# Performance work log

Measured on AMD Instinct MI355X. Metric: run time of the kernel, lower is better.

The kernel has to match this reference:

```python
import jax, jax.numpy as jnp
import numpy as np

B, H, S, DK, DV = 2, 16, 2048, 64, 64

def setup_inputs() -> dict:
    key = jax.random.key(0)
    kq, kk, kv, km = jax.random.split(key, 4)
    q = jax.random.normal(kq, (B, H, S, DK), dtype=jnp.float32)
    k = jax.random.normal(kk, (B, H, S, DK), dtype=jnp.float32)
    v = jax.random.normal(kv, (B, H, S, DV), dtype=jnp.float32)
    mask = jax.random.randint(km, (B, H, S, S), 0, 2).astype(jnp.bool_)
    return {"q": q, "k": k, "v": v, "mask": mask}

def reference(q, k, v, mask):
    d_k = q.shape[-1]
    # scores: [B, H, Sq, Sk]
    scores = jnp.einsum('bhqd,bhkd->bhqk', q, k) / np.sqrt(d_k).astype(jnp.float32)
    scores = jnp.where(mask, jnp.float32(-1e9), scores)
    attn = jax.nn.softmax(scores, axis=-1)
    return jnp.einsum('bhqk,bhkd->bhqd', attn, v)
```

## Files before the change

kernel.cpp:

```cpp
#include <hip/hip_runtime.h>


#define LOG2E 1.4426950408889634f
#define QSCALE (0.125f * LOG2E)

typedef __attribute__((ext_vector_type(8))) short short8;
typedef __attribute__((ext_vector_type(4))) short short4v;
typedef __attribute__((ext_vector_type(4))) float f32x4;
typedef unsigned __attribute__((ext_vector_type(4))) uintv4;

constexpr int S = 2048, D = 64;

__device__ __forceinline__ short bf16rne(float x) {
  union { float f; unsigned u; } cv; cv.f = x;
  unsigned u = cv.u;
  u += 0x7fffu + ((u >> 16) & 1u);
  return (short)(u >> 16);
}

__device__ __forceinline__ void glds16(const void* g, void* l) {
  __builtin_amdgcn_global_load_lds(
      (const __attribute__((address_space(1))) void*)g,
      (__attribute__((address_space(3))) void*)l, 16, 0, 0);
}

__global__ void prep(const float* __restrict__ kp, const float* __restrict__ vp,
                     short* __restrict__ kb, short* __restrict__ vt,
                     const unsigned* __restrict__ m, int* __restrict__ flag) {
  const int b = blockIdx.x;
  const int tid = threadIdx.x;
  if (b == 0 && tid < 64) {
    unsigned v = m[tid];
    unsigned long long big = __ballot(v > 1u && v != 0x3F800000u);
    unsigned long long isf = __ballot(v == 0x3F800000u);
    if (tid == 0) *flag = (big != 0ull && isf == 0ull) ? 1 : 0;
  }
  if (b < 2048) {
    size_t i = ((size_t)b * 256 + tid) * 8;
    float4 a = *(const float4*)(kp + i);
    float4 c = *(const float4*)(kp + i + 4);
    short8 s;
    s[0] = bf16rne(a.x); s[1] = bf16rne(a.y); s[2] = bf16rne(a.z); s[3] = bf16rne(a.w);
    s[4] = bf16rne(c.x); s[5] = bf16rne(c.y); s[6] = bf16rne(c.z); s[7] = bf16rne(c.w);
    *(short8*)&kb[i] = s;
  } else {
    __shared__ float tile[64][65];
    const int bb = b - 2048;
    const int bh = bb >> 5, k0 = (bb & 31) * 64;
    const float* src = vp + ((size_t)(bh * S + k0)) * D;
#pragma unroll
    for (int i = 0; i < 4; ++i) {
      int row = i * 16 + (tid >> 4);
      int col = (tid & 15) * 4;
      float4 x = *(const float4*)(src + row * D + col);
      tile[row][col] = x.x; tile[row][col + 1] = x.y;
      tile[row][col + 2] = x.z; tile[row][col + 3] = x.w;
    }
    __syncthreads();
#pragma unroll
    for (int i = 0; i < 4; ++i) {
      int dim = i * 16 + (tid >> 4);
      int kb4 = (tid & 15) * 4;
      short4v s;
#pragma unroll
      for (int j = 0; j < 4; ++j) s[j] = bf16rne(tile[kb4 + j][dim]);
      *(short4v*)&vt[((size_t)(bh * D + dim)) * S + k0 + kb4] = s;
    }
  }
}

__launch_bounds__(256, 4)
__global__ void attn_fwd(const float* __restrict__ qp, const short* __restrict__ kb,
                         const short* __restrict__ vt, const void* __restrict__ mp,
                         float* __restrict__ op, const int* __restrict__ fmtp) {
  const int fmt  = *fmtp;
  const int tid  = threadIdx.x;
  const int lane = tid & 63;
  const int w    = tid >> 6;
  const int c    = lane & 15;
  const int quad = lane >> 4;
  const int cx   = c & 7;

  const int bh = blockIdx.x >> 5;
  const int q0 = (blockIdx.x & 31) * 64;

  __shared__ short ks[2][64 * 64];
  __shared__ short vs[2][64 * 64];
  __shared__ short pst[4][16 * 64];

  const float* qg = qp + ((size_t)(bh * S + q0 + w * 16 + c)) * D;
  short8 qB[2];
#pragma unroll
  for (int kk = 0; kk < 2; ++kk) {
    const float* p = qg + kk * 32 + quad * 8;
    float4 x = *(const float4*)(p);
    float4 y = *(const float4*)(p + 4);
    short8 f;
    f[0] = bf16rne(x.x * QSCALE); f[1] = bf16rne(x.y * QSCALE);
    f[2] = bf16rne(x.z * QSCALE); f[3] = bf16rne(x.w * QSCALE);
    f[4] = bf16rne(y.x * QSCALE); f[5] = bf16rne(y.y * QSCALE);
    f[6] = bf16rne(y.z * QSCALE); f[7] = bf16rne(y.w * QSCALE);
    qB[kk] = f;
  }

  f32x4 O[4];
#pragma unroll
  for (int t = 0; t < 4; ++t) O[t] = (f32x4){0.f, 0.f, 0.f, 0.f};
  float L = 0.f;

  const int rsub = lane >> 3;
  const int csw  = (lane & 7) ^ rsub;
  const short* kbase = kb + ((size_t)(bh * S)) * D;
  const short* vbase = vt + ((size_t)(bh * D)) * S;

  const int sw0 = ((quad    ) ^ cx) * 8;
  const int sw1 = ((quad | 4) ^ cx) * 8;

  const size_t mrow = ((size_t)(bh * S + q0 + w * 16 + c)) * S;

  uintv4  mr4[4];
  unsigned mr1[4];

  auto stage = [&](int it, int buf) {
    const int k0 = it * 64;
#pragma unroll
    for (int h2 = 0; h2 < 2; ++h2) {
      const int row = (h2 * 4 + w) * 8 + rsub;
      glds16(kbase + (size_t)(k0 + row) * 64 + csw * 8,
             (char*)&ks[buf][0] + (h2 * 4 + w) * 1024);
      glds16(vbase + (size_t)row * S + k0 + csw * 8,
             (char*)&vs[buf][0] + (h2 * 4 + w) * 1024);
    }
  };

  stage(0, 0);
  if (fmt == 1) {
    const unsigned char* mq = (const unsigned char*)mp + mrow + 4 * quad;
#pragma unroll
    for (int t = 0; t < 4; ++t)
      mr1[t] = __builtin_nontemporal_load((const unsigned*)(mq + 16 * t));
  } else {
    const unsigned* mq = (const unsigned*)mp + mrow + 4 * quad;
#pragma unroll
    for (int t = 0; t < 4; ++t)
      mr4[t] = __builtin_nontemporal_load((const uintv4*)(mq + 16 * t));
  }

  for (int it = 0; it < 32; ++it) {
    const int buf = it & 1;
    __syncthreads();

    if (it + 1 < 32) stage(it + 1, buf ^ 1);

    unsigned mb[4];
    if (fmt == 1) {
#pragma unroll
      for (int t = 0; t < 4; ++t) mb[t] = mr1[t];
    } else {
#pragma unroll
      for (int t = 0; t < 4; ++t) {
        uintv4 v = mr4[t];
        mb[t] = (v[0] ? 1u : 0u) | (v[1] ? 0x100u : 0u) |
                (v[2] ? 0x10000u : 0u) | (v[3] ? 0x1000000u : 0u);
      }
    }

    if (it + 1 < 32) {
      const int k1 = (it + 1) * 64;
      if (fmt == 1) {
        const unsigned char* mq = (const unsigned char*)mp + mrow + k1 + 4 * quad;
#pragma unroll
        for (int t = 0; t < 4; ++t)
          mr1[t] = __builtin_nontemporal_load((const unsigned*)(mq + 16 * t));
      } else {
        const unsigned* mq = (const unsigned*)mp + mrow + k1 + 4 * quad;
#pragma unroll
        for (int t = 0; t < 4; ++t)
          mr4[t] = __builtin_nontemporal_load((const uintv4*)(mq + 16 * t));
      }
    }

    float part = 0.f;
#pragma unroll
    for (int t = 0; t < 4; ++t) {
      short8 ka0 = *(const short8*)&ks[buf][(16 * t + c) * 64 + sw0];
      short8 ka1 = *(const short8*)&ks[buf][(16 * t + c) * 64 + sw1];
      f32x4 z = (f32x4){0.f, 0.f, 0.f, 0.f};
      z = __builtin_amdgcn_mfma_f32_16x16x32_bf16(ka0, qB[0], z, 0, 0, 0);
      z = __builtin_amdgcn_mfma_f32_16x16x32_bf16(ka1, qB[1], z, 0, 0, 0);
      short4v s4;
#pragma unroll
      for (int r = 0; r < 4; ++r) {
        float e = ((mb[t] >> (8 * r)) & 0xffu) ? 0.f : exp2f(z[r]);
        part += e;
        s4[r] = bf16rne(e);
      }
      *(short4v*)&pst[w][c * 64 + (((2 * t + (quad >> 1)) ^ cx) << 3) +
                         ((quad & 1) << 2)] = s4;
    }

    part += __shfl_xor(part, 16);
    part += __shfl_xor(part, 32);
    L += part;

    short8 pa0 = *(const short8*)&pst[w][c * 64 + ((quad ^ cx) << 3)];
    short8 pa1 = *(const short8*)&pst[w][c * 64 + (((quad | 4) ^ cx) << 3)];
#pragma unroll
    for (int t = 0; t < 4; ++t) {
      short8 vb0 = *(const short8*)&vs[buf][(16 * t + c) * 64 + sw0];
      short8 vb1 = *(const short8*)&vs[buf][(16 * t + c) * 64 + sw1];
      O[t] = __builtin_amdgcn_mfma_f32_16x16x32_bf16(pa0, vb0, O[t], 0, 0, 0);
      O[t] = __builtin_amdgcn_mfma_f32_16x16x32_bf16(pa1, vb1, O[t], 0, 0, 0);
    }
  }

#pragma unroll
  for (int r = 0; r < 4; ++r) {
    float Lr = __shfl(L, (lane & 48) | (quad * 4 + r));
    float inv = 1.f / Lr;
    const size_t ob = ((size_t)(bh * S + q0 + w * 16 + quad * 4 + r)) * D;
#pragma unroll
    for (int t = 0; t < 4; ++t) op[ob + 16 * t + c] = O[t][r] * inv;
  }
}

extern "C" void kernel_launch(void* const* d_in, const int* in_sizes, int n_in,
                              void* d_out, int out_size, void* d_ws, size_t ws_size,
                              hipStream_t stream) {
  const float* q = (const float*)d_in[0];
  const float* k = (const float*)d_in[1];
  const float* v = (const float*)d_in[2];
  const void*  m = d_in[3];

  short* kbuf = (short*)d_ws;
  short* vtb  = (short*)((char*)d_ws + (8u << 20));
  int* flag   = (int*)((char*)d_ws + (16u << 20));

  prep<<<3072, 256, 0, stream>>>(k, v, kbuf, vtb, (const unsigned*)m, flag);
  attn_fwd<<<1024, 256, 0, stream>>>(q, kbuf, vtb, m, (float*)d_out, flag);
}
```

Measured before the change: 757.8 us.

## Split key range across waves, load K/V fragments directly, merge partials via LDS

Each block's four waves now split into two query halves and two key halves. Each wave loads K and V^T fragments straight from global memory into registers instead of staging them in shared memory with async copies and a barrier every iteration. The P fragment is built in registers by permuting K rows so that no shared-memory round trip is needed. The two key-half partial outputs and row sums are combined through LDS at the end, and block IDs are swizzled for locality. This removes per-iteration barriers and LDS traffic but drops mask prefetching and double buffering, so it relies on caches and enough occupancy to hide global latency.

Measured after the change: 781.3 us. 3.1% more time.

```diff
diff --git a/kernel.cpp b/kernel.cpp
--- a/kernel.cpp
+++ b/kernel.cpp
@@ -16,12 +16,6 @@
   unsigned u = cv.u;
   u += 0x7fffu + ((u >> 16) & 1u);
   return (short)(u >> 16);
-}
-
-__device__ __forceinline__ void glds16(const void* g, void* l) {
-  __builtin_amdgcn_global_load_lds(
-      (const __attribute__((address_space(1))) void*)g,
-      (__attribute__((address_space(3))) void*)l, 16, 0, 0);
 }
 
 __global__ void prep(const float* __restrict__ kp, const float* __restrict__ vp,
@@ -79,148 +73,149 @@
   const int w    = tid >> 6;
   const int c    = lane & 15;
   const int quad = lane >> 4;
-  const int cx   = c & 7;
-
-  const int bh = blockIdx.x >> 5;
-  const int q0 = (blockIdx.x & 31) * 64;
-
-  __shared__ short ks[2][64 * 64];
-  __shared__ short vs[2][64 * 64];
-  __shared__ short pst[4][16 * 64];
-
-  const float* qg = qp + ((size_t)(bh * S + q0 + w * 16 + c)) * D;
-  short8 qB[2];
-#pragma unroll
-  for (int kk = 0; kk < 2; ++kk) {
-    const float* p = qg + kk * 32 + quad * 8;
-    float4 x = *(const float4*)(p);
-    float4 y = *(const float4*)(p + 4);
-    short8 f;
-    f[0] = bf16rne(x.x * QSCALE); f[1] = bf16rne(x.y * QSCALE);
-    f[2] = bf16rne(x.z * QSCALE); f[3] = bf16rne(x.w * QSCALE);
-    f[4] = bf16rne(y.x * QSCALE); f[5] = bf16rne(y.y * QSCALE);
-    f[6] = bf16rne(y.z * QSCALE); f[7] = bf16rne(y.w * QSCALE);
-    qB[kk] = f;
-  }
-
-  f32x4 O[4];
-#pragma unroll
-  for (int t = 0; t < 4; ++t) O[t] = (f32x4){0.f, 0.f, 0.f, 0.f};
-  float L = 0.f;
-
-  const int rsub = lane >> 3;
-  const int csw  = (lane & 7) ^ rsub;
+  const int kh   = w & 1;
+  const int qh   = w >> 1;
+
+  const int bid = (blockIdx.x & 7) * 128 + (blockIdx.x >> 3);
+  const int bh  = bid >> 5;
+  const int q0  = (bid & 31) * 64;
+
+  __shared__ float Olds[2][32][66];
+  __shared__ float Llds[2][32];
+
+  short8 qB[2][2];
+#pragma unroll
+  for (int qg = 0; qg < 2; ++qg) {
+    const float* qg_p = qp + ((size_t)(bh * S + q0 + qh * 32 + qg * 16 + c)) * D;
+#pragma unroll
+    for (int kk = 0; kk < 2; ++kk) {
+      const float* p = qg_p + kk * 32 + quad * 8;
+      float4 x = *(const float4*)(p);
+      float4 y = *(const float4*)(p + 4);
+      short8 f;
+      f[0] = bf16rne(x.x * QSCALE); f[1] = bf16rne(x.y * QSCALE);
+      f[2] = bf16rne(x.z * QSCALE); f[3] = bf16rne(x.w * QSCALE);
+      f[4] = bf16rne(y.x * QSCALE); f[5] = bf16rne(y.y * QSCALE);
+      f[6] = bf16rne(y.z * QSCALE); f[7] = bf16rne(y.w * QSCALE);
+      qB[qg][kk] = f;
+    }
+  }
+
+  f32x4 O[2][4];
+#pragma unroll
+  for (int qg = 0; qg < 2; ++qg)
+#pragma unroll
+    for (int dt = 0; dt < 4; ++dt) O[qg][dt] = (f32x4){0.f, 0.f, 0.f, 0.f};
+  float Lp[2] = {0.f, 0.f};
+
   const short* kbase = kb + ((size_t)(bh * S)) * D;
   const short* vbase = vt + ((size_t)(bh * D)) * S;
-
-  const int sw0 = ((quad    ) ^ cx) * 8;
-  const int sw1 = ((quad | 4) ^ cx) * 8;
-
-  const size_t mrow = ((size_t)(bh * S + q0 + w * 16 + c)) * S;
-
-  uintv4  mr4[4];
-  unsigned mr1[4];
-
-  auto stage = [&](int it, int buf) {
-    const int k0 = it * 64;
-#pragma unroll
-    for (int h2 = 0; h2 < 2; ++h2) {
-      const int row = (h2 * 4 + w) * 8 + rsub;
-      glds16(kbase + (size_t)(k0 + row) * 64 + csw * 8,
-             (char*)&ks[buf][0] + (h2 * 4 + w) * 1024);
-      glds16(vbase + (size_t)row * S + k0 + csw * 8,
-             (char*)&vs[buf][0] + (h2 * 4 + w) * 1024);
-    }
-  };
-
-  stage(0, 0);
-  if (fmt == 1) {
-    const unsigned char* mq = (const unsigned char*)mp + mrow + 4 * quad;
-#pragma unroll
-    for (int t = 0; t < 4; ++t)
-      mr1[t] = __builtin_nontemporal_load((const unsigned*)(mq + 16 * t));
-  } else {
-    const unsigned* mq = (const unsigned*)mp + mrow + 4 * quad;
-#pragma unroll
-    for (int t = 0; t < 4; ++t)
-      mr4[t] = __builtin_nontemporal_load((const uintv4*)(mq + 16 * t));
-  }
-
+  const int hr0 = 8 * (c >> 2) + (c & 3);
+
+  const size_t mro0 = ((size_t)(bh * S + q0 + qh * 32 + c)) * S;
+  const size_t mro1 = mro0 + (size_t)16 * S;
+
+#pragma unroll 1
   for (int it = 0; it < 32; ++it) {
-    const int buf = it & 1;
-    __syncthreads();
-
-    if (it + 1 < 32) stage(it + 1, buf ^ 1);
-
-    unsigned mb[4];
+    const int kO = it * 64 + kh * 32;
+
+    short8 kf[2][2];
+#pragma unroll
+    for (int kt = 0; kt < 2; ++kt)
+#pragma unroll
+      for (int kk = 0; kk < 2; ++kk)
+        kf[kt][kk] = *(const short8*)(kbase +
+            (size_t)(kO + hr0 + 4 * kt) * 64 + kk * 32 + quad * 8);
+
+    short8 vf[4];
+#pragma unroll
+    for (int dt = 0; dt < 4; ++dt)
+      vf[dt] = *(const short8*)(vbase + (size_t)(dt * 16 + c) * S + kO + quad * 8);
+
+    unsigned long long mbq0, mbq1;
     if (fmt == 1) {
-#pragma unroll
-      for (int t = 0; t < 4; ++t) mb[t] = mr1[t];
+      mbq0 = *(const unsigned long long*)((const unsigned char*)mp + mro0 + kO + 8 * quad);
+      mbq1 = *(const unsigned long long*)((const unsigned char*)mp + mro1 + kO + 8 * quad);
     } else {
-#pragma unroll
-      for (int t = 0; t < 4; ++t) {
-        uintv4 v = mr4[t];
-        mb[t] = (v[0] ? 1u : 0u) | (v[1] ? 0x100u : 0u) |
-                (v[2] ? 0x10000u : 0u) | (v[3] ? 0x1000000u : 0u);
+      const unsigned* m0 = (const unsigned*)mp + mro0 + kO + 8 * quad;
+      const unsigned* m1 = (const unsigned*)mp + mro1 + kO + 8 * quad;
+      uintv4 a0 = *(const uintv4*)m0, b0 = *(const uintv4*)(m0 + 4);
+      uintv4 a1 = *(const uintv4*)m1, b1 = *(const uintv4*)(m1 + 4);
+      mbq0 = 0ull; mbq1 = 0ull;
+#pragma unroll
+      for (int j = 0; j < 4; ++j) {
+        if (a0[j]) mbq0 |= 0xffull << (8 * j);
+        if (b0[j]) mbq0 |= 0xffull << (8 * (j + 4));
+        if (a1[j]) mbq1 |= 0xffull << (8 * j);
+        if (b1[j]) mbq1 |= 0xffull << (8 * (j + 4));
       }
     }
 
-    if (it + 1 < 32) {
-      const int k1 = (it + 1) * 64;
-      if (fmt == 1) {
-        const unsigned char* mq = (const unsigned char*)mp + mrow + k1 + 4 * quad;
-#pragma unroll
-        for (int t = 0; t < 4; ++t)
-          mr1[t] = __builtin_nontemporal_load((const unsigned*)(mq + 16 * t));
-      } else {
-        const unsigned* mq = (const unsigned*)mp + mrow + k1 + 4 * quad;
-#pragma unroll
-        for (int t = 0; t < 4; ++t)
-          mr4[t] = __builtin_nontemporal_load((const uintv4*)(mq + 16 * t));
+#pragma unroll
+    for (int qg = 0; qg < 2; ++qg) {
+      const unsigned long long mbq = qg ? mbq1 : mbq0;
+      f32x4 z0 = (f32x4){0.f, 0.f, 0.f, 0.f};
+      f32x4 z1 = (f32x4){0.f, 0.f, 0.f, 0.f};
+      z0 = __builtin_amdgcn_mfma_f32_16x16x32_bf16(kf[0][0], qB[qg][0], z0, 0, 0, 0);
+      z0 = __builtin_amdgcn_mfma_f32_16x16x32_bf16(kf[0][1], qB[qg][1], z0, 0, 0, 0);
+      z1 = __builtin_amdgcn_mfma_f32_16x16x32_bf16(kf[1][0], qB[qg][0], z1, 0, 0, 0);
+      z1 = __builtin_amdgcn_mfma_f32_16x16x32_bf16(kf[1][1], qB[qg][1], z1, 0, 0, 0);
+
+      short8 pf;
+      float part = 0.f;
+#pragma unroll
+      for (int j = 0; j < 8; ++j) {
+        float zv = (j < 4) ? z0[j & 3] : z1[j & 3];
+        float e = ((mbq >> (8 * j)) & 0xffull) ? 0.f : exp2f(zv);
+        part += e;
+        pf[j] = bf16rne(e);
       }
-    }
-
-    float part = 0.f;
-#pragma unroll
-    for (int t = 0; t < 4; ++t) {
-      short8 ka0 = *(const short8*)&ks[buf][(16 * t + c) * 64 + sw0];
-      short8 ka1 = *(const short8*)&ks[buf][(16 * t + c) * 64 + sw1];
-      f32x4 z = (f32x4){0.f, 0.f, 0.f, 0.f};
-      z = __builtin_amdgcn_mfma_f32_16x16x32_bf16(ka0, qB[0], z, 0, 0, 0);
-      z = __builtin_amdgcn_mfma_f32_16x16x32_bf16(ka1, qB[1], z, 0, 0, 0);
-      short4v s4;
+      Lp[qg] += part;
+
+#pragma unroll
+      for (int dt = 0; dt < 4; ++dt)
+        O[qg][dt] = __builtin_amdgcn_mfma_f32_16x16x32_bf16(pf, vf[dt], O[qg][dt], 0, 0, 0);
+    }
+  }
+
+  float Lq[2];
+#pragma unroll
+  for (int qg = 0; qg < 2; ++qg) {
+    float t = Lp[qg];
+    t += __shfl_xor(t, 16);
+    t += __shfl_xor(t, 32);
+    Lq[qg] = t;
+  }
+
+  if (kh == 1) {
+#pragma unroll
+    for (int qg = 0; qg < 2; ++qg)
+#pragma unroll
+      for (int dt = 0; dt < 4; ++dt)
+#pragma unroll
+        for (int r = 0; r < 4; ++r)
+          Olds[qh][qg * 16 + quad * 4 + r][dt * 16 + c] = O[qg][dt][r];
+    if (quad == 0) {
+      Llds[qh][c]      = Lq[0];
+      Llds[qh][16 + c] = Lq[1];
+    }
+  }
+  __syncthreads();
+  if (kh == 0) {
+#pragma unroll
+    for (int qg = 0; qg < 2; ++qg)
 #pragma unroll
       for (int r = 0; r < 4; ++r) {
-        float e = ((mb[t] >> (8 * r)) & 0xffu) ? 0.f : exp2f(z[r]);
-        part += e;
-        s4[r] = bf16rne(e);
+        float Ls = __shfl(Lq[qg], (lane & 48) | (quad * 4 + r)) +
+                   Llds[qh][qg * 16 + quad * 4 + r];
+        float inv = 1.f / Ls;
+        const size_t ob =
+            ((size_t)(bh * S + q0 + qh * 32 + qg * 16 + quad * 4 + r)) * D;
+#pragma unroll
+        for (int dt = 0; dt < 4; ++dt)
+          op[ob + dt * 16 + c] =
+              (O[qg][dt][r] + Olds[qh][qg * 16 + quad * 4 + r][dt * 16 + c]) * inv;
       }
-      *(short4v*)&pst[w][c * 64 + (((2 * t + (quad >> 1)) ^ cx) << 3) +
-                         ((quad & 1) << 2)] = s4;
-    }
-
-    part += __shfl_xor(part, 16);
-    part += __shfl_xor(part, 32);
-    L += part;
-
-    short8 pa0 = *(const short8*)&pst[w][c * 64 + ((quad ^ cx) << 3)];
-    short8 pa1 = *(const short8*)&pst[w][c * 64 + (((quad | 4) ^ cx) << 3)];
-#pragma unroll
-    for (int t = 0; t < 4; ++t) {
-      short8 vb0 = *(const short8*)&vs[buf][(16 * t + c) * 64 + sw0];
-      short8 vb1 = *(const short8*)&vs[buf][(16 * t + c) * 64 + sw1];
-      O[t] = __builtin_amdgcn_mfma_f32_16x16x32_bf16(pa0, vb0, O[t], 0, 0, 0);
-      O[t] = __builtin_amdgcn_mfma_f32_16x16x32_bf16(pa1, vb1, O[t], 0, 0, 0);
-    }
-  }
-
-#pragma unroll
-  for (int r = 0; r < 4; ++r) {
-    float Lr = __shfl(L, (lane & 48) | (quad * 4 + r));
-    float inv = 1.f / Lr;
-    const size_t ob = ((size_t)(bh * S + q0 + w * 16 + quad * 4 + r)) * D;
-#pragma unroll
-    for (int t = 0; t < 4; ++t) op[ob + 16 * t + c] = O[t][r] * inv;
   }
 }
 
```

## Keep softmax probabilities in registers by permuting key rows of the QK MFMA

Applied to the files above, without the earlier changes.

Reorders which key rows each lane's QK^T MFMA output covers so the resulting probabilities already sit in the register layout the PV MFMA expects as its A operand. This removes the per-wave LDS staging buffer for P, along with its stores and reloads. To make that work, the K tile swizzle is changed per wave and the mask is loaded as two 64-bit words per lane matching the new column mapping. The risk is that the more intricate index arithmetic and swizzle could introduce bank conflicts or mapping errors, and it adds some register pressure.

Result: no change. 751.5 us (-0.8%).

```diff
diff --git a/kernel.cpp b/kernel.cpp
--- a/kernel.cpp
+++ b/kernel.cpp
@@ -79,14 +79,12 @@
   const int w    = tid >> 6;
   const int c    = lane & 15;
   const int quad = lane >> 4;
-  const int cx   = c & 7;
 
   const int bh = blockIdx.x >> 5;
   const int q0 = (blockIdx.x & 31) * 64;
 
   __shared__ short ks[2][64 * 64];
   __shared__ short vs[2][64 * 64];
-  __shared__ short pst[4][16 * 64];
 
   const float* qg = qp + ((size_t)(bh * S + q0 + w * 16 + c)) * D;
   short8 qB[2];
@@ -109,42 +107,56 @@
   float L = 0.f;
 
   const int rsub = lane >> 3;
-  const int csw  = (lane & 7) ^ rsub;
+  const int cswV = (lane & 7) ^ rsub;
+  const int cswK = cswV ^ ((w & 1) << 2);
   const short* kbase = kb + ((size_t)(bh * S)) * D;
   const short* vbase = vt + ((size_t)(bh * D)) * S;
 
-  const int sw0 = ((quad    ) ^ cx) * 8;
-  const int sw1 = ((quad | 4) ^ cx) * 8;
+  const int sw0 = ((quad    ) ^ (c & 7)) * 8;
+  const int sw1 = ((quad | 4) ^ (c & 7)) * 8;
+  const int kx  = (((c >> 2) & 1) << 2);
 
   const size_t mrow = ((size_t)(bh * S + q0 + w * 16 + c)) * S;
 
-  uintv4  mr4[4];
-  unsigned mr1[4];
+  unsigned long long mm0, mm1;
 
   auto stage = [&](int it, int buf) {
     const int k0 = it * 64;
 #pragma unroll
     for (int h2 = 0; h2 < 2; ++h2) {
       const int row = (h2 * 4 + w) * 8 + rsub;
-      glds16(kbase + (size_t)(k0 + row) * 64 + csw * 8,
+      glds16(kbase + (size_t)(k0 + row) * 64 + cswK * 8,
              (char*)&ks[buf][0] + (h2 * 4 + w) * 1024);
-      glds16(vbase + (size_t)row * S + k0 + csw * 8,
+      glds16(vbase + (size_t)row * S + k0 + cswV * 8,
              (char*)&vs[buf][0] + (h2 * 4 + w) * 1024);
     }
   };
 
+  auto mload = [&](int it) {
+    const int kO = it * 64;
+    if (fmt == 1) {
+      const unsigned char* mq = (const unsigned char*)mp + mrow + kO + 8 * quad;
+      mm0 = __builtin_nontemporal_load((const unsigned long long*)mq);
+      mm1 = __builtin_nontemporal_load((const unsigned long long*)(mq + 32));
+    } else {
+#pragma unroll
+      for (int h = 0; h < 2; ++h) {
+        const unsigned* m0 = (const unsigned*)mp + mrow + kO + h * 32 + 8 * quad;
+        uintv4 a = __builtin_nontemporal_load((const uintv4*)m0);
+        uintv4 b = __builtin_nontemporal_load((const uintv4*)(m0 + 4));
+        unsigned long long t = 0ull;
+#pragma unroll
+        for (int j = 0; j < 4; ++j) {
+          if (a[j]) t |= 0xffull << (8 * j);
+          if (b[j]) t |= 0xffull << (8 * (j + 4));
+        }
+        if (h == 0) mm0 = t; else mm1 = t;
+      }
+    }
+  };
+
   stage(0, 0);
-  if (fmt == 1) {
-    const unsigned char* mq = (const unsigned char*)mp + mrow + 4 * quad;
-#pragma unroll
-    for (int t = 0; t < 4; ++t)
-      mr1[t] = __builtin_nontemporal_load((const unsigned*)(mq + 16 * t));
-  } else {
-    const unsigned* mq = (const unsigned*)mp + mrow + 4 * quad;
-#pragma unroll
-    for (int t = 0; t < 4; ++t)
-      mr4[t] = __builtin_nontemporal_load((const uintv4*)(mq + 16 * t));
-  }
+  mload(0);
 
   for (int it = 0; it < 32; ++it) {
     const int buf = it & 1;
@@ -152,59 +164,35 @@
 
     if (it + 1 < 32) stage(it + 1, buf ^ 1);
 
-    unsigned mb[4];
-    if (fmt == 1) {
-#pragma unroll
-      for (int t = 0; t < 4; ++t) mb[t] = mr1[t];
-    } else {
-#pragma unroll
-      for (int t = 0; t < 4; ++t) {
-        uintv4 v = mr4[t];
-        mb[t] = (v[0] ? 1u : 0u) | (v[1] ? 0x100u : 0u) |
-                (v[2] ? 0x10000u : 0u) | (v[3] ? 0x1000000u : 0u);
-      }
-    }
-
-    if (it + 1 < 32) {
-      const int k1 = (it + 1) * 64;
-      if (fmt == 1) {
-        const unsigned char* mq = (const unsigned char*)mp + mrow + k1 + 4 * quad;
-#pragma unroll
-        for (int t = 0; t < 4; ++t)
-          mr1[t] = __builtin_nontemporal_load((const unsigned*)(mq + 16 * t));
-      } else {
-        const unsigned* mq = (const unsigned*)mp + mrow + k1 + 4 * quad;
-#pragma unroll
-        for (int t = 0; t < 4; ++t)
-          mr4[t] = __builtin_nontemporal_load((const uintv4*)(mq + 16 * t));
-      }
-    }
-
+    const unsigned long long mb0 = mm0, mb1 = mm1;
+    if (it + 1 < 32) mload(it + 1);
+
+    short8 pa0, pa1;
     float part = 0.f;
 #pragma unroll
-    for (int t = 0; t < 4; ++t) {
-      short8 ka0 = *(const short8*)&ks[buf][(16 * t + c) * 64 + sw0];
-      short8 ka1 = *(const short8*)&ks[buf][(16 * t + c) * 64 + sw1];
+    for (int g = 0; g < 4; ++g) {
+      const int r7 = (c & 3) + 4 * (g & 1);
+      const int rr = ((g & 2) << 4) + 8 * (c >> 2) + r7;
+      const int px = ((quad ^ r7 ^ kx)) * 8;
+      short8 ka0 = *(const short8*)&ks[buf][rr * 64 + px];
+      short8 ka1 = *(const short8*)&ks[buf][rr * 64 + (px ^ 32)];
       f32x4 z = (f32x4){0.f, 0.f, 0.f, 0.f};
       z = __builtin_amdgcn_mfma_f32_16x16x32_bf16(ka0, qB[0], z, 0, 0, 0);
       z = __builtin_amdgcn_mfma_f32_16x16x32_bf16(ka1, qB[1], z, 0, 0, 0);
-      short4v s4;
+      const unsigned long long mq = (g & 2) ? mb1 : mb0;
 #pragma unroll
       for (int r = 0; r < 4; ++r) {
-        float e = ((mb[t] >> (8 * r)) & 0xffu) ? 0.f : exp2f(z[r]);
+        const int j = 4 * (g & 1) + r;
+        float e = ((mq >> (8 * j)) & 0xffull) ? 0.f : exp2f(z[r]);
         part += e;
-        s4[r] = bf16rne(e);
+        if (g & 2) pa1[j] = bf16rne(e); else pa0[j] = bf16rne(e);
       }
-      *(short4v*)&pst[w][c * 64 + (((2 * t + (quad >> 1)) ^ cx) << 3) +
-                         ((quad & 1) << 2)] = s4;
     }
 
     part += __shfl_xor(part, 16);
     part += __shfl_xor(part, 32);
     L += part;
 
-    short8 pa0 = *(const short8*)&pst[w][c * 64 + ((quad ^ cx) << 3)];
-    short8 pa1 = *(const short8*)&pst[w][c * 64 + (((quad | 4) ^ cx) << 3)];
 #pragma unroll
     for (int t = 0; t < 4; ++t) {
       short8 vb0 = *(const short8*)&vs[buf][(16 * t + c) * 64 + sw0];
```
